# Performance work log

Measured on AMD Instinct MI355X. Metric: run time of the kernel, lower is better.

Reference implementation:

```python
import jax, jax.numpy as jnp
import numpy as np

N_HEADS = 16


def setup_inputs() -> dict:
    key = jax.random.key(0)
    ks = jax.random.split(key, 10)
    B, M, N, C, D = 2, 2048, 2048, 1024, 1024
    s = 0.02
    return {
        "kv": jax.random.normal(ks[0], (B, M, C), jnp.float32),
        "q": jax.random.normal(ks[1], (B, N, D), jnp.float32),
        "Wk": jax.random.normal(ks[2], (C, D), jnp.float32) * s,
        "bk": jnp.zeros((D,), jnp.float32),
        "Wq": jax.random.normal(ks[3], (D, D), jnp.float32) * s,
        "bq": jnp.zeros((D,), jnp.float32),
        "Wv": jax.random.normal(ks[4], (C, D), jnp.float32) * s,
        "bv": jnp.zeros((D,), jnp.float32),
        "Wp": jax.random.normal(ks[5], (D, D), jnp.float32) * s,
        "bp": jnp.zeros((D,), jnp.float32),
    }


def reference(kv, q, Wk, bk, Wq, bq, Wv, bv, Wp, bp):
    B, M, C = kv.shape
    B2, N, D = q.shape
    H = N_HEADS
    hd = D // H
    # projections (weights stored as [in, out]; torch Linear is x @ W.T + b with W [out,in])
    k = (kv @ Wk + bk).reshape(B, M, H, hd).transpose(0, 2, 1, 3)  # [B,H,M,hd]
    qh = (q @ Wq + bq).reshape(B, N, H, hd).transpose(0, 2, 1, 3)  # [B,H,N,hd]
    v = (kv @ Wv + bv).reshape(B, M, H, hd).transpose(0, 2, 1, 3)  # [B,H,M,hd]
    scale = 1.0 / jnp.sqrt(jnp.asarray(hd, k.dtype))
    att = jnp.einsum("bhnd,bhmd->bhnm", qh, k) * scale
    att = jax.nn.softmax(att, axis=-1)
    y = jnp.einsum("bhnm,bhmd->bhnd", att, v)  # [B,H,N,hd]
    y = y.transpose(0, 2, 1, 3).reshape(B, N, D)
    return y @ Wp + bp
```

## Files before the change

### kernel.cpp

```cpp
#include <hip/hip_runtime.h>

#define DV 1024
#define HD 64

typedef short v4s __attribute__((ext_vector_type(4)));
typedef short v8s __attribute__((ext_vector_type(8)));
typedef float v4f __attribute__((ext_vector_type(4)));
typedef int   v2i __attribute__((ext_vector_type(2)));

__device__ __forceinline__ short f2bf(float x){
  unsigned u = __float_as_uint(x);
  u += 0x7FFFu + ((u >> 16) & 1u);
  return (short)(u >> 16);
}

__device__ __forceinline__ int swz(int lane){
  return (((lane & 7) ^ (lane >> 3)) << 3);
}

__global__ __launch_bounds__(256) void cvt2(const float* __restrict__ xa,
                                            const float* __restrict__ xb,
                                            short* __restrict__ ya,
                                            short* __restrict__ yb, int n){
  const float* x = blockIdx.y ? xb : xa;
  short* y = blockIdx.y ? yb : ya;
  int stride = gridDim.x * 256 * 4;
  for (int i = (blockIdx.x * 256 + threadIdx.x) * 4; i < n; i += stride){
    float4 v = *(const float4*)(x + i);
    v4s s; s.x = f2bf(v.x); s.y = f2bf(v.y); s.z = f2bf(v.z); s.w = f2bf(v.w);
    *(v4s*)(y + i) = s;
  }
}

__global__ __launch_bounds__(256) void tcvt4(
    const float* __restrict__ W0, const float* __restrict__ W1,
    const float* __restrict__ W2, const float* __restrict__ W3,
    short* __restrict__ T0, short* __restrict__ T1,
    short* __restrict__ T2, short* __restrict__ T3){
  const float* W; short* Wt;
  switch (blockIdx.z){
    case 0: W = W0; Wt = T0; break;
    case 1: W = W1; Wt = T1; break;
    case 2: W = W2; Wt = T2; break;
    default: W = W3; Wt = T3; break;
  }
  __shared__ short L[64 * 68];
  const int t = threadIdx.x;
  const int k0 = blockIdx.y * 64, n0 = blockIdx.x * 64;
  const int rr = t >> 4, cc = (t & 15) * 4;
  #pragma unroll
  for (int j = 0; j < 4; j++){
    int r = rr + j * 16;
    float4 v = *(const float4*)(W + (size_t)(k0 + r) * DV + n0 + cc);
    v4s s; s.x = f2bf(v.x); s.y = f2bf(v.y); s.z = f2bf(v.z); s.w = f2bf(v.w);
    *(v4s*)&L[r * 68 + cc] = s;
  }
  __syncthreads();
  #pragma unroll
  for (int j = 0; j < 4; j++){
    int n = rr + j * 16;
    v4s s;
    s.x = L[(cc + 0) * 68 + n];
    s.y = L[(cc + 1) * 68 + n];
    s.z = L[(cc + 2) * 68 + n];
    s.w = L[(cc + 3) * 68 + n];
    *(v4s*)(Wt + (size_t)(n0 + n) * DV + k0 + cc) = s;
  }
}

template<typename OUT_T>
__device__ __forceinline__ void gemm_tile(
    const short* __restrict__ A, const short* __restrict__ Bt,
    const float* __restrict__ bias, OUT_T* __restrict__ C,
    int M, int N, int K, float out_scale, int m0, int n0, bool bias_row)
{
  __shared__ short As[128 * 64];
  __shared__ short Bs[128 * 64];
  const int tid = threadIdx.x;
  const int wave = tid >> 6, lane = tid & 63;
  const int quad = lane >> 4, l15 = lane & 15;
  const int wr = (wave >> 1) * 64, wc = (wave & 1) * 64;
  const int srow = lane >> 3;
  const int sw = swz(lane);
  const v4f vzero = {0.f, 0.f, 0.f, 0.f};

  const short* pa[4]; const short* pb[4];
  #pragma unroll
  for (int ii = 0; ii < 4; ii++){
    int i = wave * 4 + ii;
    pa[ii] = A  + (size_t)(m0 + i * 8 + srow) * K + sw;
    pb[ii] = Bt + (size_t)(n0 + i * 8 + srow) * K + sw;
  }

  v8s ra[4], rb[4];
  #pragma unroll
  for (int ii = 0; ii < 4; ii++){
    ra[ii] = *(const v8s*)(pa[ii]);
    rb[ii] = *(const v8s*)(pb[ii]);
  }

  v4f acc[4][4];
  #pragma unroll
  for (int i = 0; i < 4; i++)
    #pragma unroll
    for (int j = 0; j < 4; j++)
      acc[i][j] = vzero;

  for (int kt = 0; kt < K; kt += 64){
    __syncthreads();
    #pragma unroll
    for (int ii = 0; ii < 4; ii++){
      int i = wave * 4 + ii;
      *(v8s*)&As[i * 512 + lane * 8] = ra[ii];
      *(v8s*)&Bs[i * 512 + lane * 8] = rb[ii];
    }
    __syncthreads();
    if (kt + 64 < K){
      #pragma unroll
      for (int ii = 0; ii < 4; ii++){
        ra[ii] = *(const v8s*)(pa[ii] + kt + 64);
        rb[ii] = *(const v8s*)(pb[ii] + kt + 64);
      }
    }
    #pragma unroll
    for (int ks = 0; ks < 2; ks++){
      v8s a[4], b[4];
      #pragma unroll
      for (int mt = 0; mt < 4; mt++)
        a[mt] = *(const v8s*)&As[(wr + mt * 16 + l15) * 64 + (((ks * 4 + quad) ^ (l15 & 7)) << 3)];
      #pragma unroll
      for (int nt = 0; nt < 4; nt++)
        b[nt] = *(const v8s*)&Bs[(wc + nt * 16 + l15) * 64 + (((ks * 4 + quad) ^ (l15 & 7)) << 3)];
      #pragma unroll
      for (int mt = 0; mt < 4; mt++)
        #pragma unroll
        for (int nt = 0; nt < 4; nt++)
          acc[mt][nt] = __builtin_amdgcn_mfma_f32_16x16x32_bf16(a[mt], b[nt], acc[mt][nt], 0, 0, 0);
    }
  }

  #pragma unroll
  for (int mt = 0; mt < 4; mt++){
    #pragma unroll
    for (int nt = 0; nt < 4; nt++){
      int row = m0 + wr + mt * 16 + quad * 4;
      int col = n0 + wc + nt * 16 + l15;
      float bcol = bias_row ? 0.0f : bias[col];
      #pragma unroll
      for (int r = 0; r < 4; r++){
        float bv = bias_row ? bias[row + r] : bcol;
        float v = (acc[mt][nt][r] + bv) * out_scale;
        if (sizeof(OUT_T) == 2)
          ((short*)C)[(size_t)(row + r) * N + col] = f2bf(v);
        else
          ((float*)C)[(size_t)(row + r) * N + col] = v;
      }
    }
  }
}

__global__ __launch_bounds__(256, 3) void proj3(
    const short* __restrict__ qb, const short* __restrict__ kvb,
    const short* __restrict__ Wqt, const short* __restrict__ Wkt,
    const short* __restrict__ Wvt,
    const float* __restrict__ bq, const float* __restrict__ bk,
    const float* __restrict__ bv,
    short* __restrict__ Qp, short* __restrict__ Kp, short* __restrict__ VT,
    float qscale)
{
  int bid = blockIdx.x;
  const short *A, *Bt; const float* bias; short* C;
  int M, N, m0, n0; float scale; bool brow;
  if (bid < 512){
    int z = bid >> 8, l = bid & 255;
    M = 4096; N = 1024; m0 = (l & 31) * 128; n0 = (l >> 5) * 128;
    A = z ? kvb : qb; Bt = z ? Wkt : Wqt; bias = z ? bk : bq;
    C = z ? Kp : Qp; scale = z ? 1.0f : qscale; brow = false;
  } else {
    int l = bid - 512;
    M = 1024; N = 4096; m0 = (l >> 5) * 128; n0 = (l & 31) * 128;
    A = Wvt; Bt = kvb; bias = bv; C = VT; scale = 1.0f; brow = true;
  }
  gemm_tile<short>(A, Bt, bias, C, M, N, 1024, scale, m0, n0, brow);
}

__global__ __launch_bounds__(256, 2) void gemm_f32(
    const short* __restrict__ A, const short* __restrict__ Bt,
    const float* __restrict__ bias, float* __restrict__ C)
{
  __shared__ short As[128 * 64];
  __shared__ short Bs[64 * 64];
  const int tid = threadIdx.x;
  const int wave = tid >> 6, lane = tid & 63;
  const int quad = lane >> 4, l15 = lane & 15;
  const int bid = blockIdx.x;
  const int m0 = (bid & 31) * 128, n0 = (bid >> 5) * 64;
  const int wr = (wave >> 1) * 64, wc = (wave & 1) * 32;
  const int srow = lane >> 3;
  const int sw = swz(lane);
  const int K = 1024;
  const v4f vzero = {0.f, 0.f, 0.f, 0.f};

  const short* pa[4]; const short* pb[2];
  #pragma unroll
  for (int ii = 0; ii < 4; ii++)
    pa[ii] = A + (size_t)(m0 + (wave * 4 + ii) * 8 + srow) * K + sw;
  #pragma unroll
  for (int ii = 0; ii < 2; ii++)
    pb[ii] = Bt + (size_t)(n0 + (wave * 2 + ii) * 8 + srow) * K + sw;

  v8s ra[4], rb[2];
  #pragma unroll
  for (int ii = 0; ii < 4; ii++) ra[ii] = *(const v8s*)(pa[ii]);
  #pragma unroll
  for (int ii = 0; ii < 2; ii++) rb[ii] = *(const v8s*)(pb[ii]);

  v4f acc[4][2];
  #pragma unroll
  for (int i = 0; i < 4; i++){ acc[i][0] = vzero; acc[i][1] = vzero; }

  for (int kt = 0; kt < K; kt += 64){
    __syncthreads();
    #pragma unroll
    for (int ii = 0; ii < 4; ii++)
      *(v8s*)&As[(wave * 4 + ii) * 512 + lane * 8] = ra[ii];
    #pragma unroll
    for (int ii = 0; ii < 2; ii++)
      *(v8s*)&Bs[(wave * 2 + ii) * 512 + lane * 8] = rb[ii];
    __syncthreads();
    if (kt + 64 < K){
      #pragma unroll
      for (int ii = 0; ii < 4; ii++) ra[ii] = *(const v8s*)(pa[ii] + kt + 64);
      #pragma unroll
      for (int ii = 0; ii < 2; ii++) rb[ii] = *(const v8s*)(pb[ii] + kt + 64);
    }
    #pragma unroll
    for (int ks = 0; ks < 2; ks++){
      v8s a[4], b[2];
      #pragma unroll
      for (int mt = 0; mt < 4; mt++)
        a[mt] = *(const v8s*)&As[(wr + mt * 16 + l15) * 64 + (((ks * 4 + quad) ^ (l15 & 7)) << 3)];
      #pragma unroll
      for (int nt = 0; nt < 2; nt++)
        b[nt] = *(const v8s*)&Bs[(wc + nt * 16 + l15) * 64 + (((ks * 4 + quad) ^ (l15 & 7)) << 3)];
      #pragma unroll
      for (int mt = 0; mt < 4; mt++)
        #pragma unroll
        for (int nt = 0; nt < 2; nt++)
          acc[mt][nt] = __builtin_amdgcn_mfma_f32_16x16x32_bf16(a[mt], b[nt], acc[mt][nt], 0, 0, 0);
    }
  }

  #pragma unroll
  for (int mt = 0; mt < 4; mt++){
    #pragma unroll
    for (int nt = 0; nt < 2; nt++){
      int row = m0 + wr + mt * 16 + quad * 4;
      int col = n0 + wc + nt * 16 + l15;
      float bcol = bias[col];
      #pragma unroll
      for (int r = 0; r < 4; r++)
        C[(size_t)(row + r) * 1024 + col] = acc[mt][nt][r] + bcol;
    }
  }
}

__global__ __launch_bounds__(256, 3) void attn(
    const short* __restrict__ Qp, const short* __restrict__ Kp,
    const short* __restrict__ Vt, short* __restrict__ Y)
{
  __shared__ short Ks[64 * 64];
  __shared__ short Vs[64 * 68];
  const int tid = threadIdx.x;
  const int wave = tid >> 6, lane = tid & 63;
  const int quad = lane >> 4, l15 = lane & 15;
  const int gid = blockIdx.x;
  const int qi = gid >> 5, bh = gid & 31;
  const int h = bh & 15, b = bh >> 4;
  const int n0 = qi * 128;
  const int srow = lane >> 3;
  const int c8 = (lane & 7) * 8;
  const int sw = swz(lane);
  const size_t rowbase = (size_t)b * 2048;
  const v4f vzero = {0.f, 0.f, 0.f, 0.f};

  v8s qf[2][2];
  #pragma unroll
  for (int qt = 0; qt < 2; qt++){
    const short* qrow = Qp + (rowbase + n0 + wave * 32 + qt * 16 + l15) * DV + h * HD + quad * 8;
    qf[qt][0] = *(const v8s*)(qrow);
    qf[qt][1] = *(const v8s*)(qrow + 32);
  }

  const short* pk[2]; const short* pv[2];
  #pragma unroll
  for (int ii = 0; ii < 2; ii++){
    int i = wave * 2 + ii;
    pk[ii] = Kp + (rowbase + i * 8 + srow) * DV + h * HD + sw;
    pv[ii] = Vt + (size_t)(h * HD + i * 8 + srow) * 4096 + rowbase + c8;
  }
  v8s rk[2], rv[2];
  #pragma unroll
  for (int ii = 0; ii < 2; ii++){ rk[ii] = *(const v8s*)(pk[ii]); rv[ii] = *(const v8s*)(pv[ii]); }

  v4f o[4][2];
  #pragma unroll
  for (int dt = 0; dt < 4; dt++){ o[dt][0] = vzero; o[dt][1] = vzero; }
  float lsum[2] = {0.0f, 0.0f};

  for (int kt = 0; kt < 32; kt++){
    __syncthreads();
    #pragma unroll
    for (int ii = 0; ii < 2; ii++){
      int i = wave * 2 + ii;
      *(v8s*)&Ks[i * 512 + lane * 8] = rk[ii];
      *(v8s*)&Vs[(i * 8 + srow) * 68 + c8] = rv[ii];
    }
    __syncthreads();
    if (kt < 31){
      #pragma unroll
      for (int ii = 0; ii < 2; ii++){
        rk[ii] = *(const v8s*)(pk[ii] + (size_t)(kt + 1) * 64 * DV);
        rv[ii] = *(const v8s*)(pv[ii] + (kt + 1) * 64);
      }
    }

    v4f s[2][4];
    #pragma unroll
    for (int qt = 0; qt < 2; qt++)
      #pragma unroll
      for (int kvt = 0; kvt < 4; kvt++) s[qt][kvt] = vzero;
    #pragma unroll
    for (int ks = 0; ks < 2; ks++){
      v8s a[4];
      #pragma unroll
      for (int kvt = 0; kvt < 4; kvt++)
        a[kvt] = *(const v8s*)&Ks[(kvt * 16 + l15) * 64 + (((ks * 4 + quad) ^ (l15 & 7)) << 3)];
      #pragma unroll
      for (int kvt = 0; kvt < 4; kvt++)
        #pragma unroll
        for (int qt = 0; qt < 2; qt++)
          s[qt][kvt] = __builtin_amdgcn_mfma_f32_16x16x32_bf16(a[kvt], qf[qt][ks], s[qt][kvt], 0, 0, 0);
    }

    v4s pf[2][4];
    #pragma unroll
    for (int qt = 0; qt < 2; qt++)
      #pragma unroll
      for (int kvt = 0; kvt < 4; kvt++){
        float p0 = __builtin_amdgcn_exp2f(s[qt][kvt][0]);
        float p1 = __builtin_amdgcn_exp2f(s[qt][kvt][1]);
        float p2 = __builtin_amdgcn_exp2f(s[qt][kvt][2]);
        float p3 = __builtin_amdgcn_exp2f(s[qt][kvt][3]);
        lsum[qt] += (p0 + p1) + (p2 + p3);
        unsigned u0 = __float_as_uint(p0) + 0x8000u;
        unsigned u1 = __float_as_uint(p1) + 0x8000u;
        unsigned u2 = __float_as_uint(p2) + 0x8000u;
        unsigned u3 = __float_as_uint(p3) + 0x8000u;
        v2i pi;
        pi.x = (int)__builtin_amdgcn_perm(u1, u0, 0x07060302u);
        pi.y = (int)__builtin_amdgcn_perm(u3, u2, 0x07060302u);
        pf[qt][kvt] = __builtin_bit_cast(v4s, pi);
      }

    #pragma unroll
    for (int ks = 0; ks < 4; ks++){
      v4s a[4];
      #pragma unroll
      for (int dt = 0; dt < 4; dt++)
        a[dt] = *(const v4s*)&Vs[(dt * 16 + l15) * 68 + ks * 16 + quad * 4];
      #pragma unroll
      for (int dt = 0; dt < 4; dt++)
        #pragma unroll
        for (int qt = 0; qt < 2; qt++)
          o[dt][qt] = __builtin_amdgcn_mfma_f32_16x16x16bf16_1k(a[dt], pf[qt][ks], o[dt][qt], 0, 0, 0);
    }
  }

  #pragma unroll
  for (int qt = 0; qt < 2; qt++){
    float ls = lsum[qt];
    ls += __shfl_xor(ls, 16);
    ls += __shfl_xor(ls, 32);
    float inv = 1.0f / ls;
    size_t row = rowbase + n0 + wave * 32 + qt * 16 + l15;
    #pragma unroll
    for (int dt = 0; dt < 4; dt++){
      int col = h * HD + dt * 16 + quad * 4;
      unsigned p0 = (unsigned short)f2bf(o[dt][qt][0] * inv) |
                    ((unsigned)(unsigned short)f2bf(o[dt][qt][1] * inv) << 16);
      unsigned p1 = (unsigned short)f2bf(o[dt][qt][2] * inv) |
                    ((unsigned)(unsigned short)f2bf(o[dt][qt][3] * inv) << 16);
      *(unsigned*)(Y + row * DV + col)     = p0;
      *(unsigned*)(Y + row * DV + col + 2) = p1;
    }
  }
}

extern "C" void kernel_launch(void* const* d_in, const int* in_sizes, int n_in,
                              void* d_out, int out_size, void* d_ws, size_t ws_size,
                              hipStream_t stream) {
  const float* kv = (const float*)d_in[0];
  const float* q  = (const float*)d_in[1];
  const float* Wk = (const float*)d_in[2];
  const float* bk = (const float*)d_in[3];
  const float* Wq = (const float*)d_in[4];
  const float* bq = (const float*)d_in[5];
  const float* Wv = (const float*)d_in[6];
  const float* bv = (const float*)d_in[7];
  const float* Wp = (const float*)d_in[8];
  const float* bp = (const float*)d_in[9];

  const size_t E  = 4194304;
  const size_t WE = 1048576;
  short* p   = (short*)d_ws;
  short* kvb = p; p += E;
  short* qb  = p; p += E;
  short* Wkt = p; p += WE;
  short* Wqt = p; p += WE;
  short* Wvt = p; p += WE;
  short* Wpt = p; p += WE;
  short* Kp  = p; p += E;
  short* Qp  = p; p += E;
  short* VT  = p; p += E;
  short* Yb  = p; p += E;

  cvt2<<<dim3(512, 2), 256, 0, stream>>>(kv, q, kvb, qb, (int)E);
  tcvt4<<<dim3(16, 16, 4), 256, 0, stream>>>(Wk, Wq, Wv, Wp, Wkt, Wqt, Wvt, Wpt);

  proj3<<<768, 256, 0, stream>>>(qb, kvb, Wqt, Wkt, Wvt, bq, bk, bv,
                                 Qp, Kp, VT, 0.18033688011f);

  attn<<<512, 256, 0, stream>>>(Qp, Kp, VT, Yb);

  gemm_f32<<<512, 256, 0, stream>>>(Yb, Wpt, bp, (float*)d_out);
}
```

Baseline: 204.8 us.

## Double-buffer shared memory in output GEMM and attention kernels

Both the final projection GEMM and the attention kernel now use two LDS buffers. Each iteration writes the next tile into the spare buffer and prefetches the tile after that from global memory, then computes from the current buffer. This cuts the two barriers per iteration down to one. The cost is twice the LDS footprint, and attention occupancy is lowered to 2 blocks per CU via launch bounds.

Result: no change. 207.1 us (+1.1%).

```diff
diff --git a/kernel.cpp b/kernel.cpp
--- a/kernel.cpp
+++ b/kernel.cpp
@@ -188,8 +188,8 @@
     const short* __restrict__ A, const short* __restrict__ Bt,
     const float* __restrict__ bias, float* __restrict__ C)
 {
-  __shared__ short As[128 * 64];
-  __shared__ short Bs[64 * 64];
+  __shared__ short As[2][128 * 64];
+  __shared__ short Bs[2][64 * 64];
   const int tid = threadIdx.x;
   const int wave = tid >> 6, lane = tid & 63;
   const int quad = lane >> 4, l15 = lane & 15;
@@ -214,41 +214,54 @@
   for (int ii = 0; ii < 4; ii++) ra[ii] = *(const v8s*)(pa[ii]);
   #pragma unroll
   for (int ii = 0; ii < 2; ii++) rb[ii] = *(const v8s*)(pb[ii]);
+  #pragma unroll
+  for (int ii = 0; ii < 4; ii++)
+    *(v8s*)&As[0][(wave * 4 + ii) * 512 + lane * 8] = ra[ii];
+  #pragma unroll
+  for (int ii = 0; ii < 2; ii++)
+    *(v8s*)&Bs[0][(wave * 2 + ii) * 512 + lane * 8] = rb[ii];
+  #pragma unroll
+  for (int ii = 0; ii < 4; ii++) ra[ii] = *(const v8s*)(pa[ii] + 64);
+  #pragma unroll
+  for (int ii = 0; ii < 2; ii++) rb[ii] = *(const v8s*)(pb[ii] + 64);
+  __syncthreads();
 
   v4f acc[4][2];
   #pragma unroll
   for (int i = 0; i < 4; i++){ acc[i][0] = vzero; acc[i][1] = vzero; }
 
-  for (int kt = 0; kt < K; kt += 64){
-    __syncthreads();
-    #pragma unroll
-    for (int ii = 0; ii < 4; ii++)
-      *(v8s*)&As[(wave * 4 + ii) * 512 + lane * 8] = ra[ii];
-    #pragma unroll
-    for (int ii = 0; ii < 2; ii++)
-      *(v8s*)&Bs[(wave * 2 + ii) * 512 + lane * 8] = rb[ii];
-    __syncthreads();
-    if (kt + 64 < K){
-      #pragma unroll
-      for (int ii = 0; ii < 4; ii++) ra[ii] = *(const v8s*)(pa[ii] + kt + 64);
-      #pragma unroll
-      for (int ii = 0; ii < 2; ii++) rb[ii] = *(const v8s*)(pb[ii] + kt + 64);
+  for (int it = 0; it < 16; it++){
+    const int cur = it & 1, nxt = cur ^ 1;
+    if (it < 15){
+      #pragma unroll
+      for (int ii = 0; ii < 4; ii++)
+        *(v8s*)&As[nxt][(wave * 4 + ii) * 512 + lane * 8] = ra[ii];
+      #pragma unroll
+      for (int ii = 0; ii < 2; ii++)
+        *(v8s*)&Bs[nxt][(wave * 2 + ii) * 512 + lane * 8] = rb[ii];
+      if (it < 14){
+        #pragma unroll
+        for (int ii = 0; ii < 4; ii++) ra[ii] = *(const v8s*)(pa[ii] + (it + 2) * 64);
+        #pragma unroll
+        for (int ii = 0; ii < 2; ii++) rb[ii] = *(const v8s*)(pb[ii] + (it + 2) * 64);
+      }
     }
     #pragma unroll
     for (int ks = 0; ks < 2; ks++){
       v8s a[4], b[2];
       #pragma unroll
       for (int mt = 0; mt < 4; mt++)
-        a[mt] = *(const v8s*)&As[(wr + mt * 16 + l15) * 64 + (((ks * 4 + quad) ^ (l15 & 7)) << 3)];
+        a[mt] = *(const v8s*)&As[cur][(wr + mt * 16 + l15) * 64 + (((ks * 4 + quad) ^ (l15 & 7)) << 3)];
       #pragma unroll
       for (int nt = 0; nt < 2; nt++)
-        b[nt] = *(const v8s*)&Bs[(wc + nt * 16 + l15) * 64 + (((ks * 4 + quad) ^ (l15 & 7)) << 3)];
+        b[nt] = *(const v8s*)&Bs[cur][(wc + nt * 16 + l15) * 64 + (((ks * 4 + quad) ^ (l15 & 7)) << 3)];
       #pragma unroll
       for (int mt = 0; mt < 4; mt++)
         #pragma unroll
         for (int nt = 0; nt < 2; nt++)
           acc[mt][nt] = __builtin_amdgcn_mfma_f32_16x16x32_bf16(a[mt], b[nt], acc[mt][nt], 0, 0, 0);
     }
+    __syncthreads();
   }
 
   #pragma unroll
@@ -265,12 +278,12 @@
   }
 }
 
-__global__ __launch_bounds__(256, 3) void attn(
+__global__ __launch_bounds__(256, 2) void attn(
     const short* __restrict__ Qp, const short* __restrict__ Kp,
     const short* __restrict__ Vt, short* __restrict__ Y)
 {
-  __shared__ short Ks[64 * 64];
-  __shared__ short Vs[64 * 68];
+  __shared__ short Ks[2][64 * 64];
+  __shared__ short Vs[2][64 * 68];
   const int tid = threadIdx.x;
   const int wave = tid >> 6, lane = tid & 63;
   const int quad = lane >> 4, l15 = lane & 15;
@@ -299,9 +312,22 @@
     pk[ii] = Kp + (rowbase + i * 8 + srow) * DV + h * HD + sw;
     pv[ii] = Vt + (size_t)(h * HD + i * 8 + srow) * 4096 + rowbase + c8;
   }
+
   v8s rk[2], rv[2];
   #pragma unroll
   for (int ii = 0; ii < 2; ii++){ rk[ii] = *(const v8s*)(pk[ii]); rv[ii] = *(const v8s*)(pv[ii]); }
+  #pragma unroll
+  for (int ii = 0; ii < 2; ii++){
+    int i = wave * 2 + ii;
+    *(v8s*)&Ks[0][i * 512 + lane * 8] = rk[ii];
+    *(v8s*)&Vs[0][(i * 8 + srow) * 68 + c8] = rv[ii];
+  }
+  #pragma unroll
+  for (int ii = 0; ii < 2; ii++){
+    rk[ii] = *(const v8s*)(pk[ii] + (size_t)64 * DV);
+    rv[ii] = *(const v8s*)(pv[ii] + 64);
+  }
+  __syncthreads();
 
   v4f o[4][2];
   #pragma unroll
@@ -309,19 +335,20 @@
   float lsum[2] = {0.0f, 0.0f};
 
   for (int kt = 0; kt < 32; kt++){
-    __syncthreads();
-    #pragma unroll
-    for (int ii = 0; ii < 2; ii++){
-      int i = wave * 2 + ii;
-      *(v8s*)&Ks[i * 512 + lane * 8] = rk[ii];
-      *(v8s*)&Vs[(i * 8 + srow) * 68 + c8] = rv[ii];
-    }
-    __syncthreads();
+    const int cur = kt & 1, nxt = cur ^ 1;
     if (kt < 31){
       #pragma unroll
       for (int ii = 0; ii < 2; ii++){
-        rk[ii] = *(const v8s*)(pk[ii] + (size_t)(kt + 1) * 64 * DV);
-        rv[ii] = *(const v8s*)(pv[ii] + (kt + 1) * 64);
+        int i = wave * 2 + ii;
+        *(v8s*)&Ks[nxt][i * 512 + lane * 8] = rk[ii];
+        *(v8s*)&Vs[nxt][(i * 8 + srow) * 68 + c8] = rv[ii];
+      }
+      if (kt < 30){
+        #pragma unroll
+        for (int ii = 0; ii < 2; ii++){
+          rk[ii] = *(const v8s*)(pk[ii] + (size_t)(kt + 2) * 64 * DV);
+          rv[ii] = *(const v8s*)(pv[ii] + (kt + 2) * 64);
+        }
       }
     }
 
@@ -335,7 +362,7 @@
       v8s a[4];
       #pragma unroll
       for (int kvt = 0; kvt < 4; kvt++)
-        a[kvt] = *(const v8s*)&Ks[(kvt * 16 + l15) * 64 + (((ks * 4 + quad) ^ (l15 & 7)) << 3)];
+        a[kvt] = *(const v8s*)&Ks[cur][(kvt * 16 + l15) * 64 + (((ks * 4 + quad) ^ (l15 & 7)) << 3)];
       #pragma unroll
       for (int kvt = 0; kvt < 4; kvt++)
         #pragma unroll
@@ -368,13 +395,14 @@
       v4s a[4];
       #pragma unroll
       for (int dt = 0; dt < 4; dt++)
-        a[dt] = *(const v4s*)&Vs[(dt * 16 + l15) * 68 + ks * 16 + quad * 4];
+        a[dt] = *(const v4s*)&Vs[cur][(dt * 16 + l15) * 68 + ks * 16 + quad * 4];
       #pragma unroll
       for (int dt = 0; dt < 4; dt++)
         #pragma unroll
         for (int qt = 0; qt < 2; qt++)
           o[dt][qt] = __builtin_amdgcn_mfma_f32_16x16x16bf16_1k(a[dt], pf[qt][ks], o[dt][qt], 0, 0, 0);
     }
+    __syncthreads();
   }
 
   #pragma unroll
```

## Split attention over two KV halves, double-buffer LDS, and add reduction kernel

Applied to the files above, without the earlier changes.

The attention kernel now splits each (batch, head, query-tile) over two halves of the key/value sequence, which doubles the grid to 1024 blocks to improve CU occupancy. Each half writes an unnormalized bf16 partial output and its row sums into reused workspace. A new reduce kernel adds the two partials and normalizes them. The K/V LDS tiles are double-buffered so each iteration needs one barrier instead of two, and launch bounds are raised to 4 blocks per CU. The cost is an extra kernel launch, extra global traffic for the partials, and an extra bf16 rounding of each partial before they are summed.

Measured after the change: 214.6 us. +4.8%, slower.

```diff
diff --git a/kernel.cpp b/kernel.cpp
--- a/kernel.cpp
+++ b/kernel.cpp
@@ -12,6 +12,9 @@
   unsigned u = __float_as_uint(x);
   u += 0x7FFFu + ((u >> 16) & 1u);
   return (short)(u >> 16);
+}
+__device__ __forceinline__ float bf2f(short x){
+  return __uint_as_float(((unsigned)(unsigned short)x) << 16);
 }
 
 __device__ __forceinline__ int swz(int lane){
@@ -265,23 +268,27 @@
   }
 }
 
-__global__ __launch_bounds__(256, 3) void attn(
+__global__ __launch_bounds__(256, 4) void attn(
     const short* __restrict__ Qp, const short* __restrict__ Kp,
-    const short* __restrict__ Vt, short* __restrict__ Y)
+    const short* __restrict__ Vt, short* __restrict__ Pa,
+    float* __restrict__ Lw)
 {
-  __shared__ short Ks[64 * 64];
-  __shared__ short Vs[64 * 68];
+  __shared__ short Ks[2][64 * 64];
+  __shared__ short Vs[2][64 * 68];
   const int tid = threadIdx.x;
   const int wave = tid >> 6, lane = tid & 63;
   const int quad = lane >> 4, l15 = lane & 15;
   const int gid = blockIdx.x;
-  const int qi = gid >> 5, bh = gid & 31;
+  const int bh = gid & 31;
+  const int rest = gid >> 5;
+  const int qi = rest >> 1, half = rest & 1;
   const int h = bh & 15, b = bh >> 4;
   const int n0 = qi * 128;
   const int srow = lane >> 3;
   const int c8 = (lane & 7) * 8;
   const int sw = swz(lane);
   const size_t rowbase = (size_t)b * 2048;
+  const size_t kvbase = rowbase + half * 1024;
   const v4f vzero = {0.f, 0.f, 0.f, 0.f};
 
   v8s qf[2][2];
@@ -296,32 +303,46 @@
   #pragma unroll
   for (int ii = 0; ii < 2; ii++){
     int i = wave * 2 + ii;
-    pk[ii] = Kp + (rowbase + i * 8 + srow) * DV + h * HD + sw;
-    pv[ii] = Vt + (size_t)(h * HD + i * 8 + srow) * 4096 + rowbase + c8;
-  }
+    pk[ii] = Kp + (kvbase + i * 8 + srow) * DV + h * HD + sw;
+    pv[ii] = Vt + (size_t)(h * HD + i * 8 + srow) * 4096 + kvbase + c8;
+  }
+
   v8s rk[2], rv[2];
   #pragma unroll
   for (int ii = 0; ii < 2; ii++){ rk[ii] = *(const v8s*)(pk[ii]); rv[ii] = *(const v8s*)(pv[ii]); }
+  #pragma unroll
+  for (int ii = 0; ii < 2; ii++){
+    int i = wave * 2 + ii;
+    *(v8s*)&Ks[0][i * 512 + lane * 8] = rk[ii];
+    *(v8s*)&Vs[0][(i * 8 + srow) * 68 + c8] = rv[ii];
+  }
+  #pragma unroll
+  for (int ii = 0; ii < 2; ii++){
+    rk[ii] = *(const v8s*)(pk[ii] + (size_t)64 * DV);
+    rv[ii] = *(const v8s*)(pv[ii] + 64);
+  }
+  __syncthreads();
 
   v4f o[4][2];
   #pragma unroll
   for (int dt = 0; dt < 4; dt++){ o[dt][0] = vzero; o[dt][1] = vzero; }
   float lsum[2] = {0.0f, 0.0f};
 
-  for (int kt = 0; kt < 32; kt++){
-    __syncthreads();
-    #pragma unroll
-    for (int ii = 0; ii < 2; ii++){
-      int i = wave * 2 + ii;
-      *(v8s*)&Ks[i * 512 + lane * 8] = rk[ii];
-      *(v8s*)&Vs[(i * 8 + srow) * 68 + c8] = rv[ii];
-    }
-    __syncthreads();
-    if (kt < 31){
+  for (int kt = 0; kt < 16; kt++){
+    const int cur = kt & 1, nxt = cur ^ 1;
+    if (kt < 15){
       #pragma unroll
       for (int ii = 0; ii < 2; ii++){
-        rk[ii] = *(const v8s*)(pk[ii] + (size_t)(kt + 1) * 64 * DV);
-        rv[ii] = *(const v8s*)(pv[ii] + (kt + 1) * 64);
+        int i = wave * 2 + ii;
+        *(v8s*)&Ks[nxt][i * 512 + lane * 8] = rk[ii];
+        *(v8s*)&Vs[nxt][(i * 8 + srow) * 68 + c8] = rv[ii];
+      }
+      if (kt < 14){
+        #pragma unroll
+        for (int ii = 0; ii < 2; ii++){
+          rk[ii] = *(const v8s*)(pk[ii] + (size_t)(kt + 2) * 64 * DV);
+          rv[ii] = *(const v8s*)(pv[ii] + (kt + 2) * 64);
+        }
       }
     }
 
@@ -335,7 +356,7 @@
       v8s a[4];
       #pragma unroll
       for (int kvt = 0; kvt < 4; kvt++)
-        a[kvt] = *(const v8s*)&Ks[(kvt * 16 + l15) * 64 + (((ks * 4 + quad) ^ (l15 & 7)) << 3)];
+        a[kvt] = *(const v8s*)&Ks[cur][(kvt * 16 + l15) * 64 + (((ks * 4 + quad) ^ (l15 & 7)) << 3)];
       #pragma unroll
       for (int kvt = 0; kvt < 4; kvt++)
         #pragma unroll
@@ -368,33 +389,55 @@
       v4s a[4];
       #pragma unroll
       for (int dt = 0; dt < 4; dt++)
-        a[dt] = *(const v4s*)&Vs[(dt * 16 + l15) * 68 + ks * 16 + quad * 4];
+        a[dt] = *(const v4s*)&Vs[cur][(dt * 16 + l15) * 68 + ks * 16 + quad * 4];
       #pragma unroll
       for (int dt = 0; dt < 4; dt++)
         #pragma unroll
         for (int qt = 0; qt < 2; qt++)
           o[dt][qt] = __builtin_amdgcn_mfma_f32_16x16x16bf16_1k(a[dt], pf[qt][ks], o[dt][qt], 0, 0, 0);
     }
-  }
-
+    __syncthreads();
+  }
+
+  short* Po = Pa + (size_t)half * 4194304;
   #pragma unroll
   for (int qt = 0; qt < 2; qt++){
     float ls = lsum[qt];
     ls += __shfl_xor(ls, 16);
     ls += __shfl_xor(ls, 32);
-    float inv = 1.0f / ls;
-    size_t row = rowbase + n0 + wave * 32 + qt * 16 + l15;
+    int rowq = n0 + wave * 32 + qt * 16 + l15;
+    if (quad == 0)
+      Lw[half * 65536 + (bh << 11) + rowq] = ls;
+    size_t row = rowbase + rowq;
     #pragma unroll
     for (int dt = 0; dt < 4; dt++){
       int col = h * HD + dt * 16 + quad * 4;
-      unsigned p0 = (unsigned short)f2bf(o[dt][qt][0] * inv) |
-                    ((unsigned)(unsigned short)f2bf(o[dt][qt][1] * inv) << 16);
-      unsigned p1 = (unsigned short)f2bf(o[dt][qt][2] * inv) |
-                    ((unsigned)(unsigned short)f2bf(o[dt][qt][3] * inv) << 16);
-      *(unsigned*)(Y + row * DV + col)     = p0;
-      *(unsigned*)(Y + row * DV + col + 2) = p1;
-    }
-  }
+      unsigned p0 = (unsigned short)f2bf(o[dt][qt][0]) |
+                    ((unsigned)(unsigned short)f2bf(o[dt][qt][1]) << 16);
+      unsigned p1 = (unsigned short)f2bf(o[dt][qt][2]) |
+                    ((unsigned)(unsigned short)f2bf(o[dt][qt][3]) << 16);
+      *(unsigned*)(Po + row * DV + col)     = p0;
+      *(unsigned*)(Po + row * DV + col + 2) = p1;
+    }
+  }
+}
+
+__global__ __launch_bounds__(256) void attn_reduce(
+    const short* __restrict__ Pa, const float* __restrict__ Lw,
+    short* __restrict__ Yb)
+{
+  int u = blockIdx.x * 256 + threadIdx.x;
+  int row = u >> 7;
+  int colu = (u & 127) << 3;
+  int lidx = ((row >> 11) * 16 + (colu >> 6)) * 2048 + (row & 2047);
+  float inv = 1.0f / (Lw[lidx] + Lw[65536 + lidx]);
+  v8s a0 = *(const v8s*)(Pa + (size_t)row * 1024 + colu);
+  v8s a1 = *(const v8s*)(Pa + 4194304 + (size_t)row * 1024 + colu);
+  v8s y;
+  #pragma unroll
+  for (int i = 0; i < 8; i++)
+    y[i] = f2bf((bf2f(a0[i]) + bf2f(a1[i])) * inv);
+  *(v8s*)(Yb + (size_t)row * 1024 + colu) = y;
 }
 
 extern "C" void kernel_launch(void* const* d_in, const int* in_sizes, int n_in,
@@ -431,7 +474,11 @@
   proj3<<<768, 256, 0, stream>>>(qb, kvb, Wqt, Wkt, Wvt, bq, bk, bv,
                                  Qp, Kp, VT, 0.18033688011f);
 
-  attn<<<512, 256, 0, stream>>>(Qp, Kp, VT, Yb);
+  short* Pa = kvb;
+  float* Lw = (float*)Wkt;
+
+  attn<<<1024, 256, 0, stream>>>(Qp, Kp, VT, Pa, Lw);
+  attn_reduce<<<2048, 256, 0, stream>>>(Pa, Lw, Yb);
 
   gemm_f32<<<512, 256, 0, stream>>>(Yb, Wpt, bp, (float*)d_out);
 }
```

## Triple-buffer K/V tiles and software-pipeline QK^T ahead of PV in attention

Applied to the files above, without the earlier changes.

The attention kernel now keeps three K/V tiles in shared memory, so it needs one barrier per iteration instead of two. It also computes the next tile's QK^T scores before the current tile's PV matmul, so the exp/softmax work and the MFMAs of neighbouring tiles can overlap. The costs are roughly triple the LDS use (about 51KB per block) and more live registers. The launch-bounds occupancy hint drops from 3 to 2 blocks per CU to allow for this.

Result: no change. 206.8 us (+1.0%).

```diff
diff --git a/kernel.cpp b/kernel.cpp
--- a/kernel.cpp
+++ b/kernel.cpp
@@ -265,12 +265,12 @@
   }
 }
 
-__global__ __launch_bounds__(256, 3) void attn(
+__global__ __launch_bounds__(256, 2) void attn(
     const short* __restrict__ Qp, const short* __restrict__ Kp,
     const short* __restrict__ Vt, short* __restrict__ Y)
 {
-  __shared__ short Ks[64 * 64];
-  __shared__ short Vs[64 * 68];
+  __shared__ short Ks[3][64 * 64];
+  __shared__ short Vs[3][64 * 68];
   const int tid = threadIdx.x;
   const int wave = tid >> 6, lane = tid & 63;
   const int quad = lane >> 4, l15 = lane & 15;
@@ -299,49 +299,64 @@
     pk[ii] = Kp + (rowbase + i * 8 + srow) * DV + h * HD + sw;
     pv[ii] = Vt + (size_t)(h * HD + i * 8 + srow) * 4096 + rowbase + c8;
   }
+
   v8s rk[2], rv[2];
   #pragma unroll
   for (int ii = 0; ii < 2; ii++){ rk[ii] = *(const v8s*)(pk[ii]); rv[ii] = *(const v8s*)(pv[ii]); }
+  #pragma unroll
+  for (int ii = 0; ii < 2; ii++){
+    int i = wave * 2 + ii;
+    *(v8s*)&Ks[0][i * 512 + lane * 8] = rk[ii];
+    *(v8s*)&Vs[0][(i * 8 + srow) * 68 + c8] = rv[ii];
+  }
+  #pragma unroll
+  for (int ii = 0; ii < 2; ii++){
+    rk[ii] = *(const v8s*)(pk[ii] + (size_t)64 * DV);
+    rv[ii] = *(const v8s*)(pv[ii] + 64);
+  }
+  __syncthreads();
+
+  v4f s[2][4];
+  #pragma unroll
+  for (int qt = 0; qt < 2; qt++)
+    #pragma unroll
+    for (int kvt = 0; kvt < 4; kvt++) s[qt][kvt] = vzero;
+  #pragma unroll
+  for (int ks = 0; ks < 2; ks++){
+    v8s a[4];
+    #pragma unroll
+    for (int kvt = 0; kvt < 4; kvt++)
+      a[kvt] = *(const v8s*)&Ks[0][(kvt * 16 + l15) * 64 + (((ks * 4 + quad) ^ (l15 & 7)) << 3)];
+    #pragma unroll
+    for (int kvt = 0; kvt < 4; kvt++)
+      #pragma unroll
+      for (int qt = 0; qt < 2; qt++)
+        s[qt][kvt] = __builtin_amdgcn_mfma_f32_16x16x32_bf16(a[kvt], qf[qt][ks], s[qt][kvt], 0, 0, 0);
+  }
 
   v4f o[4][2];
   #pragma unroll
   for (int dt = 0; dt < 4; dt++){ o[dt][0] = vzero; o[dt][1] = vzero; }
   float lsum[2] = {0.0f, 0.0f};
 
-  for (int kt = 0; kt < 32; kt++){
+  int cur = 0, nxt = 1, nx2 = 2;
+  for (int t = 0; t < 32; t++){
+    if (t < 31){
+      #pragma unroll
+      for (int ii = 0; ii < 2; ii++){
+        int i = wave * 2 + ii;
+        *(v8s*)&Ks[nxt][i * 512 + lane * 8] = rk[ii];
+        *(v8s*)&Vs[nxt][(i * 8 + srow) * 68 + c8] = rv[ii];
+      }
+      if (t < 30){
+        #pragma unroll
+        for (int ii = 0; ii < 2; ii++){
+          rk[ii] = *(const v8s*)(pk[ii] + (size_t)(t + 2) * 64 * DV);
+          rv[ii] = *(const v8s*)(pv[ii] + (t + 2) * 64);
+        }
+      }
+    }
     __syncthreads();
-    #pragma unroll
-    for (int ii = 0; ii < 2; ii++){
-      int i = wave * 2 + ii;
-      *(v8s*)&Ks[i * 512 + lane * 8] = rk[ii];
-      *(v8s*)&Vs[(i * 8 + srow) * 68 + c8] = rv[ii];
-    }
-    __syncthreads();
-    if (kt < 31){
-      #pragma unroll
-      for (int ii = 0; ii < 2; ii++){
-        rk[ii] = *(const v8s*)(pk[ii] + (size_t)(kt + 1) * 64 * DV);
-        rv[ii] = *(const v8s*)(pv[ii] + (kt + 1) * 64);
-      }
-    }
-
-    v4f s[2][4];
-    #pragma unroll
-    for (int qt = 0; qt < 2; qt++)
-      #pragma unroll
-      for (int kvt = 0; kvt < 4; kvt++) s[qt][kvt] = vzero;
-    #pragma unroll
-    for (int ks = 0; ks < 2; ks++){
-      v8s a[4];
-      #pragma unroll
-      for (int kvt = 0; kvt < 4; kvt++)
-        a[kvt] = *(const v8s*)&Ks[(kvt * 16 + l15) * 64 + (((ks * 4 + quad) ^ (l15 & 7)) << 3)];
-      #pragma unroll
-      for (int kvt = 0; kvt < 4; kvt++)
-        #pragma unroll
-        for (int qt = 0; qt < 2; qt++)
-          s[qt][kvt] = __builtin_amdgcn_mfma_f32_16x16x32_bf16(a[kvt], qf[qt][ks], s[qt][kvt], 0, 0, 0);
-    }
 
     v4s pf[2][4];
     #pragma unroll
@@ -363,18 +378,39 @@
         pf[qt][kvt] = __builtin_bit_cast(v4s, pi);
       }
 
+    if (t < 31){
+      #pragma unroll
+      for (int qt = 0; qt < 2; qt++)
+        #pragma unroll
+        for (int kvt = 0; kvt < 4; kvt++) s[qt][kvt] = vzero;
+      #pragma unroll
+      for (int ks = 0; ks < 2; ks++){
+        v8s a[4];
+        #pragma unroll
+        for (int kvt = 0; kvt < 4; kvt++)
+          a[kvt] = *(const v8s*)&Ks[nxt][(kvt * 16 + l15) * 64 + (((ks * 4 + quad) ^ (l15 & 7)) << 3)];
+        #pragma unroll
+        for (int kvt = 0; kvt < 4; kvt++)
+          #pragma unroll
+          for (int qt = 0; qt < 2; qt++)
+            s[qt][kvt] = __builtin_amdgcn_mfma_f32_16x16x32_bf16(a[kvt], qf[qt][ks], s[qt][kvt], 0, 0, 0);
+      }
+    }
+
     #pragma unroll
     for (int ks = 0; ks < 4; ks++){
       v4s a[4];
       #pragma unroll
       for (int dt = 0; dt < 4; dt++)
-        a[dt] = *(const v4s*)&Vs[(dt * 16 + l15) * 68 + ks * 16 + quad * 4];
+        a[dt] = *(const v4s*)&Vs[cur][(dt * 16 + l15) * 68 + ks * 16 + quad * 4];
       #pragma unroll
       for (int dt = 0; dt < 4; dt++)
         #pragma unroll
         for (int qt = 0; qt < 2; qt++)
           o[dt][qt] = __builtin_amdgcn_mfma_f32_16x16x16bf16_1k(a[dt], pf[qt][ks], o[dt][qt], 0, 0, 0);
     }
+
+    int tmp = cur; cur = nxt; nxt = nx2; nx2 = tmp;
   }
 
   #pragma unroll
```
